# Performance work log

Hardware: AMD Instinct MI355X
Metric: run time of the kernel (lower is better)

Reference implementation:

```python
import jax, jax.numpy as jnp
import numpy as np

# graph frontier sizes per hop (neighbor-sampling style), layer i maps N[i] src -> N[i+1] dst
N = [60000, 30000, 15000, 8000]
E = [300000, 150000, 80000]
IN, H, OUT = 512, 512, 256
EPS = 1e-5


def setup_inputs() -> dict:
    key = jax.random.key(0)
    ks = jax.random.split(key, 24)
    x = jax.random.normal(ks[0], (N[0], IN), jnp.float32)
    inp = {"x": x}
    # edge indices: row0 = src idx in [0,N[i]), row1 = dst idx in [0,N[i+1])
    for i in range(3):
        src = jax.random.randint(ks[1 + 2 * i], (E[i],), 0, N[i], jnp.int32)
        dst = jax.random.randint(ks[2 + 2 * i], (E[i],), 0, N[i + 1], jnp.int32)
        inp[f"ei{i+1}"] = jnp.stack([src, dst])
    s = 0.05
    dims_in = [IN, H, H]
    for i in range(3):
        inp[f"Wl{i+1}"] = jax.random.normal(ks[7 + 4 * i], (dims_in[i], H), jnp.float32) * s
        inp[f"Wr{i+1}"] = jax.random.normal(ks[8 + 4 * i], (dims_in[i], H), jnp.float32) * s
        inp[f"g{i+1}"] = jnp.ones((H,), jnp.float32)
        inp[f"b{i+1}"] = jnp.zeros((H,), jnp.float32)
    inp["res_W"] = jax.random.normal(ks[19], (IN, H), jnp.float32) * s
    inp["res_b"] = jnp.full((H,), 0.01, jnp.float32)
    inp["mlp_W1"] = jax.random.normal(ks[20], (IN + 3 * H, 2 * OUT), jnp.float32) * s
    inp["mlp_b1"] = jnp.zeros((2 * OUT,), jnp.float32)
    inp["mlp_W2"] = jax.random.normal(ks[21], (2 * OUT, OUT), jnp.float32) * s
    inp["mlp_b2"] = jnp.zeros((OUT,), jnp.float32)
    return inp


def _sage_bn_act(x_all, ei, n_dst, Wl, Wr, g, b):
    # SAGEConv(mean aggr, bias=False): lin_l(mean_neighbors) + lin_r(x_dst)
    x_dst = x_all[:n_dst]
    msg = x_all[ei[0]]                                      # [E, d] gather
    ssum = jax.ops.segment_sum(msg, ei[1], num_segments=n_dst)
    cnt = jax.ops.segment_sum(jnp.ones((ei.shape[1], 1), x_all.dtype), ei[1], num_segments=n_dst)
    mean = ssum / jnp.maximum(cnt, 1.0)
    h = mean @ Wl + x_dst @ Wr
    mu = h.mean(axis=0)
    var = h.var(axis=0)                                     # BatchNorm1d, training-mode batch stats
    h = (h - mu) * jax.lax.rsqrt(var + EPS) * g + b
    h = jax.nn.leaky_relu(h, 0.01)
    return h, x_dst


def reference(x, ei1, ei2, ei3,
              Wl1, Wr1, g1, b1,
              Wl2, Wr2, g2, b2,
              Wl3, Wr3, g3, b3,
              res_W, res_b,
              mlp_W1, mlp_b1, mlp_W2, mlp_b2):
    end = N[3]
    collect = [x[:end]]
    # layer 1: Linear residual; torch in-place `x += res` means collected slice is post-residual
    h, x_dst = _sage_bn_act(x, ei1, N[1], Wl1, Wr1, g1, b1)
    x = h + (x_dst @ res_W + res_b)
    collect.append(x[:end])
    # layer 2: Identity residual
    h, x_dst = _sage_bn_act(x, ei2, N[2], Wl2, Wr2, g2, b2)
    x = h + x_dst
    collect.append(x[:end])
    # layer 3: Identity residual
    h, x_dst = _sage_bn_act(x, ei3, N[3], Wl3, Wr3, g3, b3)
    x = h + x_dst
    collect.append(x[:end])
    feat = jnp.concatenate(collect, axis=-1)                # [end, IN + 3H]
    z = feat @ mlp_W1 + mlp_b1                              # MLP(end_up_with_fc=True) = two plain Linears
    z = z @ mlp_W2 + mlp_b2
    return jax.nn.log_softmax(z, axis=-1)
```

## Files before the change

### kernel.cpp

```cpp
#include <hip/hip_runtime.h>

typedef __attribute__((ext_vector_type(8))) short bf16x8;
typedef __attribute__((ext_vector_type(4))) float f32x4;

static __device__ __forceinline__ short f2bf(float f) {
  union { float f; unsigned u; } v; v.f = f;
  unsigned r = v.u + 0x7fffu + ((v.u >> 16) & 1u);
  return (short)(r >> 16);
}
static __device__ __forceinline__ float bf2f(short s) {
  union { unsigned u; float f; } v; v.u = ((unsigned)(unsigned short)s) << 16;
  return v.f;
}

#define GLOBAL_AS(p) ((const __attribute__((address_space(1))) void*)(p))
#define LDS_AS(p)    ((__attribute__((address_space(3))) void*)(p))

struct WD { const float* W; short* Wt; int ldt; int koff; int Nn; };
struct PrepArgs {
  WD d[12];
  const float* x0; short* xb0; int n8;
  int* deg; int* cursor; int ndeg; float* stats; int nstats;
};

__global__ void prep_kernel(PrepArgs P) {
  int z = blockIdx.z;
  if (z < 8) {
    int gtid = (z * 256 + blockIdx.y * 16 + blockIdx.x) * 256 + threadIdx.x;
    int wv = gtid >> 6, lane = gtid & 63;
    const float4* __restrict__ src = (const float4*)P.x0;
    short4* __restrict__ dst = (short4*)P.xb0;
    int n4 = P.n8 * 2;
    for (int b = wv * 128 + lane; b < n4; b += 1048576) {
      float4 a = src[b];
      float4 c = src[b + 64];
      short4 o1; o1.x = f2bf(a.x); o1.y = f2bf(a.y); o1.z = f2bf(a.z); o1.w = f2bf(a.w);
      short4 o2; o2.x = f2bf(c.x); o2.y = f2bf(c.y); o2.z = f2bf(c.z); o2.w = f2bf(c.w);
      dst[b] = o1;
      dst[b + 64] = o2;
    }
  } else if (z == 8) {
    int base = (blockIdx.y * 16 + blockIdx.x) * 256 + threadIdx.x;
    for (int i = base; i < P.ndeg; i += 65536) { P.deg[i] = 0; P.cursor[i] = 0; }
    for (int i = base; i < P.nstats; i += 65536) P.stats[i] = 0.f;
  } else {
    __shared__ float tile[32][33];
    const WD dd = P.d[z - 9];
    int kb = blockIdx.x * 32, nb = blockIdx.y * 32;
    if (nb >= dd.Nn) return;
    int tx = threadIdx.x & 31, ty = threadIdx.x >> 5;
#pragma unroll
    for (int j = 0; j < 4; ++j) {
      int k = kb + ty + 8 * j;
      tile[ty + 8 * j][tx] = dd.W[(size_t)k * dd.Nn + nb + tx];
    }
    __syncthreads();
#pragma unroll
    for (int j = 0; j < 4; ++j) {
      int n = nb + ty + 8 * j;
      dd.Wt[(size_t)n * dd.ldt + dd.koff + kb + tx] = f2bf(tile[tx][ty + 8 * j]);
    }
  }
}

struct L3s { const int* ei[3]; int E[3]; int dbase[3]; int ebase[3]; };

__global__ void deg_all_kernel(L3s L, int* __restrict__ deg) {
  int g = blockIdx.x * 256 + threadIdx.x;
  int l = 0, e = g;
  while (l < 3 && e >= L.E[l]) { e -= L.E[l]; ++l; }
  if (l >= 3) return;
  int d = L.ei[l][L.E[l] + e];
  atomicAdd(&deg[L.dbase[l] + d], 1);
}

__global__ void scan_all_kernel(L3s Ln, const int* __restrict__ deg, int* __restrict__ offs) {
  __shared__ int sums[257];
  int l = blockIdx.x;
  int n = Ln.E[l];
  const int* dg = deg + Ln.dbase[l];
  int* of = offs + Ln.dbase[l];
  int t = threadIdx.x;
  int per = (n + 255) / 256;
  int b = t * per, e = min(b + per, n);
  int s = 0;
  for (int i = b; i < e; ++i) s += dg[i];
  sums[t] = s;
  __syncthreads();
  if (t == 0) {
    int acc = 0;
    for (int i = 0; i < 256; ++i) { int v = sums[i]; sums[i] = acc; acc += v; }
    sums[256] = acc;
  }
  __syncthreads();
  int acc = sums[t];
  for (int i = b; i < e; ++i) { of[i] = acc; acc += dg[i]; }
  if (t == 255) of[n] = sums[256];
}

__global__ void fill_all_kernel(L3s L, const int* __restrict__ offs,
                                int* __restrict__ cursor, int* __restrict__ csr) {
  int g = blockIdx.x * 256 + threadIdx.x;
  int l = 0, e = g;
  while (l < 3 && e >= L.E[l]) { e -= L.E[l]; ++l; }
  if (l >= 3) return;
  int d = L.ei[l][L.E[l] + e];
  int p = atomicAdd(&cursor[L.dbase[l] + d], 1);
  csr[L.ebase[l] + offs[L.dbase[l] + d] + p] = L.ei[l][e];
}

__global__ void aggregate_kernel(const short* __restrict__ xb, const int* __restrict__ csr,
                                 const int* __restrict__ offs, short* __restrict__ A,
                                 int n_dst) {
  int node = blockIdx.x * 4 + (threadIdx.x >> 6);
  if (node >= n_dst) return;
  int lane = threadIdx.x & 63;
  const short* xp = xb + lane * 8;
  int s0 = offs[node], s1 = offs[node + 1];
  float a[8];
#pragma unroll
  for (int j = 0; j < 8; ++j) a[j] = 0.f;
  int e = s0;
  for (; e + 3 < s1; e += 4) {
    bf16x8 v0 = *(const bf16x8*)(xp + (size_t)csr[e] * 512);
    bf16x8 v1 = *(const bf16x8*)(xp + (size_t)csr[e + 1] * 512);
    bf16x8 v2 = *(const bf16x8*)(xp + (size_t)csr[e + 2] * 512);
    bf16x8 v3 = *(const bf16x8*)(xp + (size_t)csr[e + 3] * 512);
#pragma unroll
    for (int j = 0; j < 8; ++j) a[j] += (bf2f(v0[j]) + bf2f(v1[j])) + (bf2f(v2[j]) + bf2f(v3[j]));
  }
  for (; e < s1; ++e) {
    bf16x8 v0 = *(const bf16x8*)(xp + (size_t)csr[e] * 512);
#pragma unroll
    for (int j = 0; j < 8; ++j) a[j] += bf2f(v0[j]);
  }
  float inv = (s1 > s0) ? 1.0f / (float)(s1 - s0) : 0.0f;
  bf16x8 o;
#pragma unroll
  for (int j = 0; j < 8; ++j) o[j] = f2bf(a[j] * inv);
  *(bf16x8*)(A + (size_t)node * 512 + lane * 8) = o;
}

struct G128 {
  const short* Am; const short* Ax;
  const short* Bt; int ldb;
  short* hC; float* fC; int ldc;
  int M; int K;
  const float* bias; float* stats;
  int gm; int gn;
};

__global__ __launch_bounds__(256, 4)
void gemm128_dual_kernel(G128 d0, G128 d1, int nb0) {
  __shared__ short lds[16384];
  short* As = lds;
  short* Bs = lds + 8192;
  const bool second = (int)blockIdx.x >= nb0;
  const G128& D = second ? d1 : d0;
  const int id = (int)blockIdx.x - (second ? nb0 : 0);
  const int g = id >> 3;
  const int bn = g % D.gn;
  const int bm = (g / D.gn) * 8 + (id & 7);
  if (bm >= D.gm) return;
  const int tid = threadIdx.x;
  const int wid = tid >> 6;
  const int lane = tid & 63;
  const int lm = lane & 15;
  const int quad = lane >> 4;
  const int wr = wid >> 1, wc = wid & 1;
  const int srow = lane >> 3;
  const int kswz = (((lane & 7) ^ srow) << 3);
  const int M = D.M;

  f32x4 acc[4][4];
#pragma unroll
  for (int i = 0; i < 4; ++i)
#pragma unroll
    for (int j = 0; j < 4; ++j) acc[i][j] = (f32x4)0.f;

  for (int k0 = 0; k0 < D.K; k0 += 64) {
    const short* Aptr = (k0 < 512) ? D.Am : D.Ax;
    int kloc = k0 & 511;
#pragma unroll
    for (int j = 0; j < 4; ++j) {
      int ch = wid * 4 + j;
      int arow = bm * 128 + ch * 8 + srow;
      arow = arow < M ? arow : M - 1;
      const short* ga = Aptr + (size_t)arow * 512 + kloc + kswz;
      __builtin_amdgcn_global_load_lds(GLOBAL_AS(ga), LDS_AS(As + ch * 512), 16, 0, 0);
      int brow = bn * 128 + ch * 8 + srow;
      const short* gb = D.Bt + (size_t)brow * D.ldb + k0 + kswz;
      __builtin_amdgcn_global_load_lds(GLOBAL_AS(gb), LDS_AS(Bs + ch * 512), 16, 0, 0);
    }
    __syncthreads();
#pragma unroll
    for (int ks = 0; ks < 2; ++ks) {
      bf16x8 af[4], bfr[4];
      int xo = ((ks * 4 + quad) ^ (lm & 7)) * 8;
#pragma unroll
      for (int mi = 0; mi < 4; ++mi)
        af[mi] = *(const bf16x8*)(As + (wr * 64 + mi * 16 + lm) * 64 + xo);
#pragma unroll
      for (int ni = 0; ni < 4; ++ni)
        bfr[ni] = *(const bf16x8*)(Bs + (wc * 64 + ni * 16 + lm) * 64 + xo);
#pragma unroll
      for (int mi = 0; mi < 4; ++mi)
#pragma unroll
        for (int ni = 0; ni < 4; ++ni)
          acc[mi][ni] = __builtin_amdgcn_mfma_f32_16x16x32_bf16(af[mi], bfr[ni], acc[mi][ni], 0, 0, 0);
    }
    __syncthreads();
  }

#pragma unroll
  for (int mi = 0; mi < 4; ++mi) {
#pragma unroll
    for (int ni = 0; ni < 4; ++ni) {
      int gcol = bn * 128 + wc * 64 + ni * 16 + lm;
      float bv = D.bias ? D.bias[gcol] : 0.f;
#pragma unroll
      for (int r2 = 0; r2 < 4; ++r2) {
        int grow = bm * 128 + wr * 64 + mi * 16 + quad * 4 + r2;
        if (grow < M) {
          float val = acc[mi][ni][r2] + bv;
          if (D.hC) D.hC[(size_t)grow * D.ldc + gcol] = f2bf(val);
          else      D.fC[(size_t)grow * D.ldc + gcol] = val;
        }
      }
    }
  }

  if (D.stats) {
    float* s1 = (float*)lds;
    float* s2 = s1 + 128;
    if (tid < 128) { s1[tid] = 0.f; s2[tid] = 0.f; }
    __syncthreads();
#pragma unroll
    for (int ni = 0; ni < 4; ++ni) {
      int cloc = wc * 64 + ni * 16 + lm;
      float p1 = 0.f, p2 = 0.f;
#pragma unroll
      for (int mi = 0; mi < 4; ++mi)
#pragma unroll
        for (int r2 = 0; r2 < 4; ++r2) {
          int grow = bm * 128 + wr * 64 + mi * 16 + quad * 4 + r2;
          if (grow < M) {
            float v = acc[mi][ni][r2];
            p1 += v; p2 += v * v;
          }
        }
      atomicAdd(&s1[cloc], p1);
      atomicAdd(&s2[cloc], p2);
    }
    __syncthreads();
    if (tid < 128) {
      int gcol = bn * 128 + tid;
      atomicAdd(&D.stats[gcol], s1[tid]);
      atomicAdd(&D.stats[512 + gcol], s2[tid]);
    }
  }
}

__global__ __launch_bounds__(256, 4)
void sage_gemm64_kernel(const short* __restrict__ A0, const short* __restrict__ A1,
                        const short* __restrict__ A2, const short* __restrict__ A3,
                        const short* __restrict__ Bt, int ldb,
                        short* __restrict__ hC, float* __restrict__ fC, int ldc,
                        int M, int K, const float* __restrict__ bias,
                        float* __restrict__ stats, int gm, int gn) {
  __shared__ short lds[12288];
  short* As = lds;
  short* Bs = lds + 4096;
  const int id = blockIdx.x;
  const int g = id >> 3;
  const int bn = g % gn;
  const int bm = (g / gn) * 8 + (id & 7);
  if (bm >= gm) return;
  const int tid = threadIdx.x;
  const int wid = tid >> 6;
  const int lane = tid & 63;
  const int lm = lane & 15;
  const int quad = lane >> 4;
  const int srow = lane >> 3;
  const int kswz = (((lane & 7) ^ srow) << 3);
  const short* Aps[4] = {A0, A1, A2, A3};

  f32x4 acc[4][2];
#pragma unroll
  for (int i = 0; i < 4; ++i)
#pragma unroll
    for (int j = 0; j < 2; ++j) acc[i][j] = (f32x4)0.f;

  for (int k0 = 0; k0 < K; k0 += 64) {
    const short* Aptr = Aps[k0 >> 9];
    int kloc = k0 & 511;
#pragma unroll
    for (int j = 0; j < 6; ++j) {
      int ch = wid * 6 + j;
      if (ch < 8) {
        int arow = bm * 64 + ch * 8 + srow;
        arow = arow < M ? arow : M - 1;
        const short* ga = Aptr + (size_t)arow * 512 + kloc + kswz;
        __builtin_amdgcn_global_load_lds(GLOBAL_AS(ga), LDS_AS(As + ch * 512), 16, 0, 0);
      } else {
        int bc = ch - 8;
        int brow = bn * 128 + bc * 8 + srow;
        const short* gb = Bt + (size_t)brow * ldb + k0 + kswz;
        __builtin_amdgcn_global_load_lds(GLOBAL_AS(gb), LDS_AS(Bs + bc * 512), 16, 0, 0);
      }
    }
    __syncthreads();
#pragma unroll
    for (int ks = 0; ks < 2; ++ks) {
      bf16x8 af[4], bfr[2];
      int xo = ((ks * 4 + quad) ^ (lm & 7)) * 8;
#pragma unroll
      for (int mi = 0; mi < 4; ++mi)
        af[mi] = *(const bf16x8*)(As + (mi * 16 + lm) * 64 + xo);
#pragma unroll
      for (int ni = 0; ni < 2; ++ni)
        bfr[ni] = *(const bf16x8*)(Bs + (wid * 32 + ni * 16 + lm) * 64 + xo);
#pragma unroll
      for (int mi = 0; mi < 4; ++mi)
#pragma unroll
        for (int ni = 0; ni < 2; ++ni)
          acc[mi][ni] = __builtin_amdgcn_mfma_f32_16x16x32_bf16(af[mi], bfr[ni], acc[mi][ni], 0, 0, 0);
    }
    __syncthreads();
  }

#pragma unroll
  for (int mi = 0; mi < 4; ++mi) {
#pragma unroll
    for (int ni = 0; ni < 2; ++ni) {
      int gcol = bn * 128 + wid * 32 + ni * 16 + lm;
      float bv = bias ? bias[gcol] : 0.f;
#pragma unroll
      for (int r2 = 0; r2 < 4; ++r2) {
        int grow = bm * 64 + mi * 16 + quad * 4 + r2;
        if (grow < M) {
          float val = acc[mi][ni][r2] + bv;
          if (hC) hC[(size_t)grow * ldc + gcol] = f2bf(val);
          else    fC[(size_t)grow * ldc + gcol] = val;
        }
      }
    }
  }

  if (stats) {
    float* s1 = (float*)lds;
    float* s2 = s1 + 128;
    if (tid < 128) { s1[tid] = 0.f; s2[tid] = 0.f; }
    __syncthreads();
#pragma unroll
    for (int ni = 0; ni < 2; ++ni) {
      int cloc = wid * 32 + ni * 16 + lm;
      float p1 = 0.f, p2 = 0.f;
#pragma unroll
      for (int mi = 0; mi < 4; ++mi)
#pragma unroll
        for (int r2 = 0; r2 < 4; ++r2) {
          int grow = bm * 64 + mi * 16 + quad * 4 + r2;
          if (grow < M) {
            float v = acc[mi][ni][r2];
            p1 += v; p2 += v * v;
          }
        }
      atomicAdd(&s1[cloc], p1);
      atomicAdd(&s2[cloc], p2);
    }
    __syncthreads();
    if (tid < 128) {
      int gcol = bn * 128 + tid;
      atomicAdd(&stats[gcol], s1[tid]);
      atomicAdd(&stats[512 + gcol], s2[tid]);
    }
  }
}

__global__ void apply_kernel(const short* __restrict__ h, const float* __restrict__ stats,
                             const float* __restrict__ g, const float* __restrict__ b,
                             const short* __restrict__ r, const float* __restrict__ res_b,
                             const short* __restrict__ xdst, short* __restrict__ outp,
                             int n, float inv_n) {
  int i = blockIdx.x;
  int c = threadIdx.x * 4;
  short4 hb = *(const short4*)(h + (size_t)i * 512 + c);
  float4 s1 = *(const float4*)(stats + c);
  float4 s2 = *(const float4*)(stats + 512 + c);
  float4 gv = *(const float4*)(g + c);
  float4 bv = *(const float4*)(b + c);
  float mux = s1.x * inv_n, muy = s1.y * inv_n, muz = s1.z * inv_n, muw = s1.w * inv_n;
  float rsx = rsqrtf(s2.x * inv_n - mux * mux + 1e-5f);
  float rsy = rsqrtf(s2.y * inv_n - muy * muy + 1e-5f);
  float rsz = rsqrtf(s2.z * inv_n - muz * muz + 1e-5f);
  float rsw = rsqrtf(s2.w * inv_n - muw * muw + 1e-5f);
  float4 o;
  o.x = (bf2f(hb.x) - mux) * rsx * gv.x + bv.x;
  o.y = (bf2f(hb.y) - muy) * rsy * gv.y + bv.y;
  o.z = (bf2f(hb.z) - muz) * rsz * gv.z + bv.z;
  o.w = (bf2f(hb.w) - muw) * rsw * gv.w + bv.w;
  o.x = o.x >= 0.f ? o.x : 0.01f * o.x;
  o.y = o.y >= 0.f ? o.y : 0.01f * o.y;
  o.z = o.z >= 0.f ? o.z : 0.01f * o.z;
  o.w = o.w >= 0.f ? o.w : 0.01f * o.w;
  if (r) {
    short4 rv = *(const short4*)(r + (size_t)i * 512 + c);
    float4 rb = *(const float4*)(res_b + c);
    o.x += bf2f(rv.x) + rb.x; o.y += bf2f(rv.y) + rb.y;
    o.z += bf2f(rv.z) + rb.z; o.w += bf2f(rv.w) + rb.w;
  } else {
    short4 xv = *(const short4*)(xdst + (size_t)i * 512 + c);
    o.x += bf2f(xv.x); o.y += bf2f(xv.y); o.z += bf2f(xv.z); o.w += bf2f(xv.w);
  }
  short4 ov;
  ov.x = f2bf(o.x); ov.y = f2bf(o.y); ov.z = f2bf(o.z); ov.w = f2bf(o.w);
  *(short4*)(outp + (size_t)i * 512 + c) = ov;
}

__global__ void lsm_kernel(const float* __restrict__ z, float* __restrict__ outp) {
  __shared__ float redm[4], reds[4];
  int row = blockIdx.x, t = threadIdx.x;
  float v = z[(size_t)row * 256 + t];
  float m = v;
#pragma unroll
  for (int o = 32; o >= 1; o >>= 1) m = fmaxf(m, __shfl_down(m, o, 64));
  if ((t & 63) == 0) redm[t >> 6] = m;
  __syncthreads();
  m = fmaxf(fmaxf(redm[0], redm[1]), fmaxf(redm[2], redm[3]));
  float e = __expf(v - m);
  float s = e;
#pragma unroll
  for (int o = 32; o >= 1; o >>= 1) s += __shfl_down(s, o, 64);
  if ((t & 63) == 0) reds[t >> 6] = s;
  __syncthreads();
  s = reds[0] + reds[1] + reds[2] + reds[3];
  outp[(size_t)row * 256 + t] = v - m - __logf(s);
}

extern "C" void kernel_launch(void* const* d_in, const int* in_sizes, int n_in,
                              void* d_out, int out_size, void* d_ws, size_t ws_size,
                              hipStream_t stream) {
  const float* x0 = (const float*)d_in[0];
  const int* eis[3] = {(const int*)d_in[1], (const int*)d_in[2], (const int*)d_in[3]};
  const float* Wl[3] = {(const float*)d_in[4], (const float*)d_in[8], (const float*)d_in[12]};
  const float* Wr[3] = {(const float*)d_in[5], (const float*)d_in[9], (const float*)d_in[13]};
  const float* gg[3] = {(const float*)d_in[6], (const float*)d_in[10], (const float*)d_in[14]};
  const float* bb[3] = {(const float*)d_in[7], (const float*)d_in[11], (const float*)d_in[15]};
  const float* res_W = (const float*)d_in[16];
  const float* res_b = (const float*)d_in[17];
  const float* mlp_W1 = (const float*)d_in[18];
  const float* mlp_b1 = (const float*)d_in[19];
  const float* mlp_W2 = (const float*)d_in[20];
  const float* mlp_b2 = (const float*)d_in[21];
  float* out = (float*)d_out;

  const int Ns[4] = {60000, 30000, 15000, 8000};
  int Es[3];
  for (int l = 0; l < 3; ++l) Es[l] = in_sizes[1 + l] / 2;
  int Etot = Es[0] + Es[1] + Es[2];

  char* ws = (char*)d_ws;
  size_t off = 0;
  auto alloc = [&](size_t bytes) { size_t r = off; off += (bytes + 255) & ~(size_t)255; return r; };
  short* Bt[3];
  Bt[0] = (short*)(ws + alloc(512 * 1024 * 2));
  Bt[1] = (short*)(ws + alloc(512 * 1024 * 2));
  Bt[2] = (short*)(ws + alloc(512 * 1024 * 2));
  short* Rt = (short*)(ws + alloc(512 * 512 * 2));
  short* W1t = (short*)(ws + alloc(512 * 2048 * 2));
  short* W2t = (short*)(ws + alloc(256 * 512 * 2));
  const int dbase[3] = {0, 30001, 45002};
  const int ndeg = 53003;
  int ebase[3] = {0, Es[0], Es[0] + Es[1]};
  int* deg3 = (int*)(ws + alloc((size_t)ndeg * 4));
  int* offs3 = (int*)(ws + alloc((size_t)ndeg * 4));
  int* cursor3 = (int*)(ws + alloc((size_t)ndeg * 4));
  int* csr3 = (int*)(ws + alloc((size_t)Etot * 4));
  float* stats3 = (float*)(ws + alloc(3 * 1024 * 4));
  short* xb0 = (short*)(ws + alloc((size_t)60000 * 512 * 2));
  short* x1b = (short*)(ws + alloc((size_t)30000 * 512 * 2));
  short* x2b = (short*)(ws + alloc((size_t)15000 * 512 * 2));
  short* x3b = (short*)(ws + alloc((size_t)8000 * 512 * 2));
  short* Abuf = (short*)(ws + alloc((size_t)30000 * 512 * 2));
  short* h = (short*)(ws + alloc((size_t)30000 * 512 * 2));
  size_t scr_off = alloc((size_t)30000 * 512 * 2);
  short* rbuf = (short*)(ws + scr_off);
  short* z1b = (short*)(ws + scr_off);
  float* z2 = (float*)(ws + alloc((size_t)8000 * 256 * 4));

  PrepArgs P;
  P.d[0] = {Wl[0], Bt[0], 1024, 0, 512};
  P.d[1] = {Wr[0], Bt[0], 1024, 512, 512};
  P.d[2] = {Wl[1], Bt[1], 1024, 0, 512};
  P.d[3] = {Wr[1], Bt[1], 1024, 512, 512};
  P.d[4] = {Wl[2], Bt[2], 1024, 0, 512};
  P.d[5] = {Wr[2], Bt[2], 1024, 512, 512};
  P.d[6] = {res_W, Rt, 512, 0, 512};
  P.d[7] = {mlp_W1 + 0 * 512 * 512, W1t, 2048, 0, 512};
  P.d[8] = {mlp_W1 + 1 * 512 * 512, W1t, 2048, 512, 512};
  P.d[9] = {mlp_W1 + 2 * 512 * 512, W1t, 2048, 1024, 512};
  P.d[10] = {mlp_W1 + 3 * 512 * 512, W1t, 2048, 1536, 512};
  P.d[11] = {mlp_W2, W2t, 512, 0, 256};
  P.x0 = x0; P.xb0 = xb0; P.n8 = 60000 * 512 / 8;
  P.deg = deg3; P.cursor = cursor3; P.ndeg = ndeg;
  P.stats = stats3; P.nstats = 3 * 1024;
  prep_kernel<<<dim3(16, 16, 21), 256, 0, stream>>>(P);

  L3s L;
  for (int l = 0; l < 3; ++l) {
    L.ei[l] = eis[l]; L.E[l] = Es[l]; L.dbase[l] = dbase[l]; L.ebase[l] = ebase[l];
  }
  deg_all_kernel<<<dim3((Etot + 255) / 256), 256, 0, stream>>>(L, deg3);
  L3s Ln = L;
  Ln.E[0] = Ns[1]; Ln.E[1] = Ns[2]; Ln.E[2] = Ns[3];
  scan_all_kernel<<<dim3(3), 256, 0, stream>>>(Ln, deg3, offs3);
  fill_all_kernel<<<dim3((Etot + 255) / 256), 256, 0, stream>>>(L, offs3, cursor3, csr3);

  const short* xin[3] = {xb0, x1b, x2b};
  short* xout[3] = {x1b, x2b, x3b};

  auto gblocks = [](int gm, int gn) { return ((gm + 7) / 8) * 8 * gn; };

  for (int l = 0; l < 3; ++l) {
    int n_dst = Ns[l + 1];
    float* stats = stats3 + l * 1024;
    aggregate_kernel<<<dim3((n_dst + 3) / 4), 256, 0, stream>>>(
        xin[l], csr3 + ebase[l], offs3 + dbase[l], Abuf, n_dst);
    if (l == 0) {
      int gm = (n_dst + 127) / 128;
      int nb0 = gblocks(gm, 4);
      G128 dsage = {Abuf, xin[l], Bt[l], 1024, h, nullptr, 512,
                    n_dst, 1024, nullptr, stats, gm, 4};
      G128 dres  = {xin[l], nullptr, Rt, 512, rbuf, nullptr, 512,
                    n_dst, 512, nullptr, nullptr, gm, 4};
      gemm128_dual_kernel<<<dim3(nb0 + gblocks(gm, 4)), 256, 0, stream>>>(
          dsage, dres, nb0);
    } else {
      int gm = (n_dst + 63) / 64;
      sage_gemm64_kernel<<<dim3(gblocks(gm, 4)), 256, 0, stream>>>(
          Abuf, xin[l], nullptr, nullptr, Bt[l], 1024, h, nullptr, 512, n_dst, 1024,
          nullptr, stats, gm, 4);
    }
    apply_kernel<<<dim3(n_dst), 128, 0, stream>>>(h, stats, gg[l], bb[l],
                                                  l == 0 ? rbuf : nullptr, res_b,
                                                  xin[l], xout[l], n_dst, 1.0f / n_dst);
  }

  {
    int gm = (8000 + 63) / 64;
    sage_gemm64_kernel<<<dim3(gblocks(gm, 4)), 256, 0, stream>>>(
        xb0, x1b, x2b, x3b, W1t, 2048, z1b, nullptr, 512, 8000, 2048, mlp_b1,
        nullptr, gm, 4);
    sage_gemm64_kernel<<<dim3(gblocks(gm, 2)), 256, 0, stream>>>(
        z1b, nullptr, nullptr, nullptr, W2t, 512, nullptr, z2, 256, 8000, 512,
        mlp_b2, nullptr, gm, 2);
  }
  lsm_kernel<<<dim3(8000), 256, 0, stream>>>(z2, out);
}
```

Measured before the change: 437.1 us.

## Fuse final linear with log-softmax and merge degree counting into prep kernel

```diff
diff --git a/kernel.cpp b/kernel.cpp
--- a/kernel.cpp
+++ b/kernel.cpp
@@ -16,11 +16,20 @@
 #define GLOBAL_AS(p) ((const __attribute__((address_space(1))) void*)(p))
 #define LDS_AS(p)    ((__attribute__((address_space(3))) void*)(p))
 
+struct L3s { const int* ei[3]; int E[3]; int dbase[3]; int ebase[3]; };
+
+__global__ void zero_kernel(int* __restrict__ deg, int* __restrict__ cursor,
+                            float* __restrict__ stats, int ndeg, int nstats) {
+  int base = blockIdx.x * 256 + threadIdx.x;
+  for (int i = base; i < ndeg; i += 16384) { deg[i] = 0; cursor[i] = 0; }
+  for (int i = base; i < nstats; i += 16384) stats[i] = 0.f;
+}
+
 struct WD { const float* W; short* Wt; int ldt; int koff; int Nn; };
 struct PrepArgs {
   WD d[12];
   const float* x0; short* xb0; int n8;
-  int* deg; int* cursor; int ndeg; float* stats; int nstats;
+  int* deg; L3s L;
 };
 
 __global__ void prep_kernel(PrepArgs P) {
@@ -39,13 +48,16 @@
       dst[b] = o1;
       dst[b + 64] = o2;
     }
-  } else if (z == 8) {
-    int base = (blockIdx.y * 16 + blockIdx.x) * 256 + threadIdx.x;
-    for (int i = base; i < P.ndeg; i += 65536) { P.deg[i] = 0; P.cursor[i] = 0; }
-    for (int i = base; i < P.nstats; i += 65536) P.stats[i] = 0.f;
+  } else if (z < 17) {
+    int g = (z - 8) * 65536 + (blockIdx.y * 16 + blockIdx.x) * 256 + threadIdx.x;
+    int l = 0, e = g;
+    while (l < 3 && e >= P.L.E[l]) { e -= P.L.E[l]; ++l; }
+    if (l >= 3) return;
+    int d = P.L.ei[l][P.L.E[l] + e];
+    atomicAdd(&P.deg[P.L.dbase[l] + d], 1);
   } else {
     __shared__ float tile[32][33];
-    const WD dd = P.d[z - 9];
+    const WD dd = P.d[z - 17];
     int kb = blockIdx.x * 32, nb = blockIdx.y * 32;
     if (nb >= dd.Nn) return;
     int tx = threadIdx.x & 31, ty = threadIdx.x >> 5;
@@ -61,17 +73,6 @@
       dd.Wt[(size_t)n * dd.ldt + dd.koff + kb + tx] = f2bf(tile[tx][ty + 8 * j]);
     }
   }
-}
-
-struct L3s { const int* ei[3]; int E[3]; int dbase[3]; int ebase[3]; };
-
-__global__ void deg_all_kernel(L3s L, int* __restrict__ deg) {
-  int g = blockIdx.x * 256 + threadIdx.x;
-  int l = 0, e = g;
-  while (l < 3 && e >= L.E[l]) { e -= L.E[l]; ++l; }
-  if (l >= 3) return;
-  int d = L.ei[l][L.E[l] + e];
-  atomicAdd(&deg[L.dbase[l] + d], 1);
 }
 
 __global__ void scan_all_kernel(L3s Ln, const int* __restrict__ deg, int* __restrict__ offs) {
@@ -376,6 +377,118 @@
       atomicAdd(&stats[512 + gcol], s2[tid]);
     }
   }
+}
+
+__global__ __launch_bounds__(256, 4)
+void head2_kernel(const short* __restrict__ A, const short* __restrict__ Bt,
+                  const float* __restrict__ bias, float* __restrict__ outp) {
+  __shared__ short lds[20480];
+  short* As = lds;
+  short* Bs = lds + 4096;
+  const int bm = blockIdx.x;
+  const int tid = threadIdx.x;
+  const int wid = tid >> 6;
+  const int lane = tid & 63;
+  const int lm = lane & 15;
+  const int quad = lane >> 4;
+  const int srow = lane >> 3;
+  const int kswz = (((lane & 7) ^ srow) << 3);
+
+  f32x4 acc[4][4];
+#pragma unroll
+  for (int i = 0; i < 4; ++i)
+#pragma unroll
+    for (int j = 0; j < 4; ++j) acc[i][j] = (f32x4)0.f;
+
+  for (int k0 = 0; k0 < 512; k0 += 64) {
+#pragma unroll
+    for (int j = 0; j < 10; ++j) {
+      int ch = wid * 10 + j;
+      if (ch < 8) {
+        int arow = bm * 64 + ch * 8 + srow;
+        const short* ga = A + (size_t)arow * 512 + k0 + kswz;
+        __builtin_amdgcn_global_load_lds(GLOBAL_AS(ga), LDS_AS(As + ch * 512), 16, 0, 0);
+      } else {
+        int bc = ch - 8;
+        int brow = bc * 8 + srow;
+        const short* gb = Bt + (size_t)brow * 512 + k0 + kswz;
+        __builtin_amdgcn_global_load_lds(GLOBAL_AS(gb), LDS_AS(Bs + bc * 512), 16, 0, 0);
+      }
+    }
+    __syncthreads();
+#pragma unroll
+    for (int ks = 0; ks < 2; ++ks) {
+      bf16x8 af[4], bfr[4];
+      int xo = ((ks * 4 + quad) ^ (lm & 7)) * 8;
+#pragma unroll
+      for (int mi = 0; mi < 4; ++mi)
+        af[mi] = *(const bf16x8*)(As + (mi * 16 + lm) * 64 + xo);
+#pragma unroll
+      for (int ni = 0; ni < 4; ++ni)
+        bfr[ni] = *(const bf16x8*)(Bs + (wid * 64 + ni * 16 + lm) * 64 + xo);
+#pragma unroll
+      for (int mi = 0; mi < 4; ++mi)
+#pragma unroll
+        for (int ni = 0; ni < 4; ++ni)
+          acc[mi][ni] = __builtin_amdgcn_mfma_f32_16x16x32_bf16(af[mi], bfr[ni], acc[mi][ni], 0, 0, 0);
+    }
+    __syncthreads();
+  }
+
+  float bv[4];
+#pragma unroll
+  for (int ni = 0; ni < 4; ++ni) bv[ni] = bias[wid * 64 + ni * 16 + lm];
+
+  float* red = (float*)lds;
+  float rmax[4][4];
+#pragma unroll
+  for (int mi = 0; mi < 4; ++mi)
+#pragma unroll
+    for (int r2 = 0; r2 < 4; ++r2) {
+      float m = acc[mi][0][r2] + bv[0];
+#pragma unroll
+      for (int ni = 1; ni < 4; ++ni) m = fmaxf(m, acc[mi][ni][r2] + bv[ni]);
+      m = fmaxf(m, __shfl_xor(m, 1, 64));
+      m = fmaxf(m, __shfl_xor(m, 2, 64));
+      m = fmaxf(m, __shfl_xor(m, 4, 64));
+      m = fmaxf(m, __shfl_xor(m, 8, 64));
+      rmax[mi][r2] = m;
+      if (lm == 0) red[wid * 64 + mi * 16 + quad * 4 + r2] = m;
+    }
+  __syncthreads();
+  float fm[4][4];
+#pragma unroll
+  for (int mi = 0; mi < 4; ++mi)
+#pragma unroll
+    for (int r2 = 0; r2 < 4; ++r2) {
+      int row = mi * 16 + quad * 4 + r2;
+      float m = fmaxf(fmaxf(red[row], red[64 + row]),
+                      fmaxf(red[128 + row], red[192 + row]));
+      fm[mi][r2] = m;
+      float s = 0.f;
+#pragma unroll
+      for (int ni = 0; ni < 4; ++ni) s += __expf(acc[mi][ni][r2] + bv[ni] - m);
+      s += __shfl_xor(s, 1, 64);
+      s += __shfl_xor(s, 2, 64);
+      s += __shfl_xor(s, 4, 64);
+      s += __shfl_xor(s, 8, 64);
+      if (lm == 0) red[256 + wid * 64 + row] = s;
+    }
+  __syncthreads();
+#pragma unroll
+  for (int mi = 0; mi < 4; ++mi)
+#pragma unroll
+    for (int r2 = 0; r2 < 4; ++r2) {
+      int row = mi * 16 + quad * 4 + r2;
+      float s = red[256 + row] + red[320 + row] + red[384 + row] + red[448 + row];
+      float ls = __logf(s);
+#pragma unroll
+      for (int ni = 0; ni < 4; ++ni) {
+        int gcol = wid * 64 + ni * 16 + lm;
+        outp[(size_t)(bm * 64 + row) * 256 + gcol] =
+            acc[mi][ni][r2] + bv[ni] - fm[mi][r2] - ls;
+      }
+    }
 }
 
 __global__ void apply_kernel(const short* __restrict__ h, const float* __restrict__ stats,
@@ -418,26 +531,6 @@
   *(short4*)(outp + (size_t)i * 512 + c) = ov;
 }
 
-__global__ void lsm_kernel(const float* __restrict__ z, float* __restrict__ outp) {
-  __shared__ float redm[4], reds[4];
-  int row = blockIdx.x, t = threadIdx.x;
-  float v = z[(size_t)row * 256 + t];
-  float m = v;
-#pragma unroll
-  for (int o = 32; o >= 1; o >>= 1) m = fmaxf(m, __shfl_down(m, o, 64));
-  if ((t & 63) == 0) redm[t >> 6] = m;
-  __syncthreads();
-  m = fmaxf(fmaxf(redm[0], redm[1]), fmaxf(redm[2], redm[3]));
-  float e = __expf(v - m);
-  float s = e;
-#pragma unroll
-  for (int o = 32; o >= 1; o >>= 1) s += __shfl_down(s, o, 64);
-  if ((t & 63) == 0) reds[t >> 6] = s;
-  __syncthreads();
-  s = reds[0] + reds[1] + reds[2] + reds[3];
-  outp[(size_t)row * 256 + t] = v - m - __logf(s);
-}
-
 extern "C" void kernel_launch(void* const* d_in, const int* in_sizes, int n_in,
                               void* d_out, int out_size, void* d_ws, size_t ws_size,
                               hipStream_t stream) {
@@ -487,7 +580,13 @@
   size_t scr_off = alloc((size_t)30000 * 512 * 2);
   short* rbuf = (short*)(ws + scr_off);
   short* z1b = (short*)(ws + scr_off);
-  float* z2 = (float*)(ws + alloc((size_t)8000 * 256 * 4));
+
+  L3s L;
+  for (int l = 0; l < 3; ++l) {
+    L.ei[l] = eis[l]; L.E[l] = Es[l]; L.dbase[l] = dbase[l]; L.ebase[l] = ebase[l];
+  }
+
+  zero_kernel<<<dim3(64), 256, 0, stream>>>(deg3, cursor3, stats3, ndeg, 3 * 1024);
 
   PrepArgs P;
   P.d[0] = {Wl[0], Bt[0], 1024, 0, 512};
@@ -503,15 +602,9 @@
   P.d[10] = {mlp_W1 + 3 * 512 * 512, W1t, 2048, 1536, 512};
   P.d[11] = {mlp_W2, W2t, 512, 0, 256};
   P.x0 = x0; P.xb0 = xb0; P.n8 = 60000 * 512 / 8;
-  P.deg = deg3; P.cursor = cursor3; P.ndeg = ndeg;
-  P.stats = stats3; P.nstats = 3 * 1024;
-  prep_kernel<<<dim3(16, 16, 21), 256, 0, stream>>>(P);
-
-  L3s L;
-  for (int l = 0; l < 3; ++l) {
-    L.ei[l] = eis[l]; L.E[l] = Es[l]; L.dbase[l] = dbase[l]; L.ebase[l] = ebase[l];
-  }
-  deg_all_kernel<<<dim3((Etot + 255) / 256), 256, 0, stream>>>(L, deg3);
+  P.deg = deg3; P.L = L;
+  prep_kernel<<<dim3(16, 16, 29), 256, 0, stream>>>(P);
+
   L3s Ln = L;
   Ln.E[0] = Ns[1]; Ln.E[1] = Ns[2]; Ln.E[2] = Ns[3];
   scan_all_kernel<<<dim3(3), 256, 0, stream>>>(Ln, deg3, offs3);
@@ -552,9 +645,6 @@
     sage_gemm64_kernel<<<dim3(gblocks(gm, 4)), 256, 0, stream>>>(
         xb0, x1b, x2b, x3b, W1t, 2048, z1b, nullptr, 512, 8000, 2048, mlp_b1,
         nullptr, gm, 4);
-    sage_gemm64_kernel<<<dim3(gblocks(gm, 2)), 256, 0, stream>>>(
-        z1b, nullptr, nullptr, nullptr, W2t, 512, nullptr, z2, 256, 8000, 512,
-        mlp_b2, nullptr, gm, 2);
-  }
-  lsm_kernel<<<dim3(8000), 256, 0, stream>>>(z2, out);
-}
+    head2_kernel<<<dim3(125), 256, 0, stream>>>(z1b, W2t, mlp_b2, out);
+  }
+}
```

Measured after the change: 445.4 us. About the same (+1.9%).
